# Performance work log

Hardware: AMD Instinct MI355X
Metric: run time of the kernel (lower is better)

## Reference

```python
import jax, jax.numpy as jnp
import numpy as np

NUM_EMBEDDINGS = 1024
EMBEDDING_DIM = 64
COMMITMENT_COST = 0.25


def setup_inputs() -> dict:
    key = jax.random.key(0)
    k1, k2 = jax.random.split(key)
    inputs = jax.random.normal(k1, (64, 32, 32, EMBEDDING_DIM), dtype=jnp.float32)
    # torch init is uniform(-1/K, 1/K); scale accordingly
    weight = jax.random.uniform(
        k2, (NUM_EMBEDDINGS, EMBEDDING_DIM), dtype=jnp.float32,
        minval=-1.0 / NUM_EMBEDDINGS, maxval=1.0 / NUM_EMBEDDINGS)
    return {"inputs": inputs, "weight": weight}


def reference(inputs, weight):
    input_shape = inputs.shape
    flat = inputs.reshape(-1, EMBEDDING_DIM)               # [N, D]
    distances = (jnp.sum(flat ** 2, axis=1, keepdims=True)
                 + jnp.sum(weight ** 2, axis=1)
                 - 2.0 * flat @ weight.T)                   # [N, K]
    encoding_indices = jnp.argmin(distances, axis=1)        # [N]
    # gather codes (equivalent to one-hot @ weight, but as a direct gather)
    quantized = weight[encoding_indices].reshape(input_shape)

    e_latent_loss = jnp.mean((jax.lax.stop_gradient(quantized) - inputs) ** 2)
    q_latent_loss = jnp.mean((quantized - jax.lax.stop_gradient(inputs)) ** 2)
    loss = q_latent_loss + COMMITMENT_COST * e_latent_loss

    # straight-through estimator
    quantized_ste = inputs + jax.lax.stop_gradient(quantized - inputs)

    # perplexity (equivalent to mean over the one-hot encodings)
    n_tokens = flat.shape[0]
    counts = jax.ops.segment_sum(
        jnp.ones((n_tokens,), jnp.float32), encoding_indices,
        num_segments=NUM_EMBEDDINGS)
    avg_probs = counts / n_tokens
    perplexity = jnp.exp(-jnp.sum(avg_probs * jnp.log(avg_probs + 1e-10)))

    indices_for_transformer = encoding_indices.reshape(input_shape[0], -1)
    return (loss, quantized_ste, perplexity, indices_for_transformer)
```

## Files before the change

kernel.cpp:

```cpp
#include <hip/hip_runtime.h>
#include <cstdint>
#include <cstddef>

#define N_TOKENS 65536
#define DIM 64
#define K_CODES 1024
#define NTH 256
#define NTHM 512
#define TPB 128
#define NCH 16

#define OFF_Q 1
#define OFF_PERP 4194305
#define OFF_IDX 4194306

#define MARGIN 1.5e-4f
#define HMARGIN 7.5e-5f

#define WS_LOSS   0
#define WS_FCNT   8
#define WS_COUNTS 16
#define WS_WHI    4112
#define WS_WLO    135184
#define WS_S2     266256
#define WS_FLIST  270352

typedef __attribute__((ext_vector_type(8))) short  s16x8;
typedef __attribute__((ext_vector_type(4))) float  f32x4;

__device__ __forceinline__ float fmulr(float a, float b){ return __fmul_rn(a,b); }
__device__ __forceinline__ float faddr(float a, float b){ return __fadd_rn(a,b); }

__device__ __forceinline__ unsigned short f2bf(float f) {
    unsigned u = __float_as_uint(f);
    unsigned r = u + 0x7fffu + ((u >> 16) & 1u);
    return (unsigned short)(r >> 16);
}
__device__ __forceinline__ float bf2f(unsigned short h) {
    return __uint_as_float(((unsigned)h) << 16);
}

__device__ float sumsq64_np(const float* __restrict__ p) {
    float s[16];
    #pragma unroll
    for (int l = 0; l < 16; ++l) {
        float a0 = fmulr(p[l],      p[l]);
        float a1 = fmulr(p[l + 16], p[l + 16]);
        float a2 = fmulr(p[l + 32], p[l + 32]);
        float a3 = fmulr(p[l + 48], p[l + 48]);
        s[l] = faddr(faddr(a0, a1), faddr(a2, a3));
    }
    #pragma unroll
    for (int len = 8; len >= 1; len >>= 1)
        #pragma unroll
        for (int l = 0; l < len; ++l)
            s[l] = faddr(s[l], s[l + len]);
    return s[0];
}

__device__ __forceinline__ void async_copy16(const void* g, void* l) {
    __builtin_amdgcn_global_load_lds(
        (const __attribute__((address_space(1))) void*)g,
        (__attribute__((address_space(3))) void*)l, 16, 0, 0);
}

__global__ void vq_prep(const float* __restrict__ W, unsigned short* __restrict__ Whi,
                        unsigned short* __restrict__ Wlo, float* __restrict__ s2g,
                        int* __restrict__ counts, int* __restrict__ gfcount,
                        double* __restrict__ loss_acc) {
    int gid = blockIdx.x * NTH + threadIdx.x;
    for (int e = gid; e < K_CODES * DIM; e += 16384) {
        float x = W[e];
        unsigned short hi = f2bf(x);
        unsigned short lo = f2bf(__fsub_rn(x, bf2f(hi)));
        int j = e >> 6, k = e & 63;
        int pos = j * 64 + (((k >> 3) ^ (j & 7)) << 3) + (k & 7);
        Whi[pos] = hi; Wlo[pos] = lo;
    }
    if (gid < K_CODES) { s2g[gid] = sumsq64_np(W + gid * 64); counts[gid] = 0; }
    if (gid == 0) { *loss_acc = 0.0; *gfcount = 0; }
}

__global__ __launch_bounds__(NTHM, 4)
void vq_main(const float* __restrict__ X, const float* __restrict__ W,
             const unsigned short* __restrict__ WhiG, const unsigned short* __restrict__ WloG,
             const float* __restrict__ s2g, float* __restrict__ out,
             double* __restrict__ loss_acc, int* __restrict__ counts,
             int* __restrict__ gfcount, unsigned short* __restrict__ gflist) {
    __shared__ __align__(16) unsigned short xs_hi[TPB * 64];
    __shared__ __align__(16) unsigned short xs_lo[TPB * 64];
    __shared__ __align__(16) unsigned short ws_hi[2][64 * 64];
    __shared__ __align__(16) unsigned short ws_lo[2][64 * 64];
    __shared__ __align__(16) float s2s[K_CODES];
    __shared__ float sm1[2][TPB];
    __shared__ float sm2[2][TPB];
    __shared__ int   si1[2][TPB];
    __shared__ int fidx[TPB];
    __shared__ int flist[TPB];
    __shared__ int fcount, gbaseS;
    __shared__ double lred[8];

    const int tid  = threadIdx.x;
    const int lane = tid & 63, wave = tid >> 6;
    const int quad = lane >> 4, lrow = lane & 15;
    const int tg   = wave & 3;
    const int chd  = wave >> 2;
    const int t0   = blockIdx.x * TPB;

    if (tid == 0) fcount = 0;

    {
        const char* gh = (const char*)WhiG;
        const char* gl = (const char*)WloG;
        char* lh = (char*)&ws_hi[0][0] + wave * 1024;
        char* ll = (char*)&ws_lo[0][0] + wave * 1024;
        async_copy16(gh + tid * 16, lh);
        async_copy16(gl + tid * 16, ll);
    }
    if (tid < 256) *(f32x4*)&s2s[tid * 4] = *(const f32x4*)&s2g[tid * 4];
    #pragma unroll
    for (int i = 0; i < 2; ++i) {
        int g = tid + NTHM * i;
        int t = g >> 3, kb = g & 7;
        const float* src = X + (size_t)(t0 + t) * DIM + kb * 8;
        float v[8];
        *(f32x4*)v       = *(const f32x4*)src;
        *(f32x4*)(v + 4) = *(const f32x4*)(src + 4);
        unsigned short h[8], l[8];
        #pragma unroll
        for (int k = 0; k < 8; ++k) {
            h[k] = f2bf(v[k]);
            l[k] = f2bf(__fsub_rn(v[k], bf2f(h[k])));
        }
        int base = t * 64 + ((kb ^ (t & 7)) << 3);
        *(s16x8*)&xs_hi[base] = *(s16x8*)h;
        *(s16x8*)&xs_lo[base] = *(s16x8*)l;
    }
    __syncthreads();

    s16x8 a_h0[2], a_h1[2], a_l0[2], a_l1[2];
    #pragma unroll
    for (int rt = 0; rt < 2; ++rt) {
        int tf = tg * 32 + rt * 16 + lrow;
        int sA = tf & 7;
        a_h0[rt] = *(const s16x8*)&xs_hi[tf * 64 + (((0 + quad) ^ sA) << 3)];
        a_h1[rt] = *(const s16x8*)&xs_hi[tf * 64 + (((4 + quad) ^ sA) << 3)];
        a_l0[rt] = *(const s16x8*)&xs_lo[tf * 64 + (((0 + quad) ^ sA) << 3)];
        a_l1[rt] = *(const s16x8*)&xs_lo[tf * 64 + (((4 + quad) ^ sA) << 3)];
    }

    float m1v[8], m2v[8]; int m1i[8];
    #pragma unroll
    for (int ri = 0; ri < 8; ++ri) { m1v[ri] = -3.4e38f; m2v[ri] = -3.4e38f; m1i[ri] = 0x7fffffff; }

    for (int ch = 0; ch < NCH; ++ch) {
        const int buf = ch & 1;
        if (ch < NCH - 1) {
            const char* gh = (const char*)WhiG + (ch + 1) * 8192;
            const char* gl = (const char*)WloG + (ch + 1) * 8192;
            char* lh = (char*)&ws_hi[buf ^ 1][0] + wave * 1024;
            char* ll = (char*)&ws_lo[buf ^ 1][0] + wave * 1024;
            async_copy16(gh + tid * 16, lh);
            async_copy16(gl + tid * 16, ll);
        }
        #pragma unroll
        for (int ct2 = 0; ct2 < 2; ++ct2) {
            int lc = chd * 32 + ct2 * 16 + lrow;
            int sB = lrow & 7;
            const unsigned short* bh = &ws_hi[buf][lc * 64];
            const unsigned short* bl = &ws_lo[buf][lc * 64];
            s16x8 b_h0 = *(const s16x8*)&bh[((0 + quad) ^ sB) << 3];
            s16x8 b_h1 = *(const s16x8*)&bh[((4 + quad) ^ sB) << 3];
            s16x8 b_l0 = *(const s16x8*)&bl[((0 + quad) ^ sB) << 3];
            s16x8 b_l1 = *(const s16x8*)&bl[((4 + quad) ^ sB) << 3];
            int jcode = ch * 64 + lc;
            float s2v = s2s[jcode];
            float ainit = fmulr(-0.5f, s2v);
            #pragma unroll
            for (int rt = 0; rt < 2; ++rt) {
                f32x4 acc = {ainit, ainit, ainit, ainit};
                acc = __builtin_amdgcn_mfma_f32_16x16x32_bf16(a_h0[rt], b_h0, acc, 0, 0, 0);
                acc = __builtin_amdgcn_mfma_f32_16x16x32_bf16(a_h1[rt], b_h1, acc, 0, 0, 0);
                acc = __builtin_amdgcn_mfma_f32_16x16x32_bf16(a_h0[rt], b_l0, acc, 0, 0, 0);
                acc = __builtin_amdgcn_mfma_f32_16x16x32_bf16(a_h1[rt], b_l1, acc, 0, 0, 0);
                acc = __builtin_amdgcn_mfma_f32_16x16x32_bf16(a_l0[rt], b_h0, acc, 0, 0, 0);
                acc = __builtin_amdgcn_mfma_f32_16x16x32_bf16(a_l1[rt], b_h1, acc, 0, 0, 0);
                #pragma unroll
                for (int r = 0; r < 4; ++r) {
                    float a = acc[r];
                    int ri = rt * 4 + r;
                    bool gt = a > m1v[ri];
                    float sec = gt ? m1v[ri] : a;
                    m2v[ri] = fmaxf(m2v[ri], sec);
                    m1v[ri] = gt ? a : m1v[ri];
                    m1i[ri] = gt ? jcode : m1i[ri];
                }
            }
        }
        __syncthreads();
    }

    #pragma unroll
    for (int m = 1; m <= 8; m <<= 1) {
        #pragma unroll
        for (int ri = 0; ri < 8; ++ri) {
            float o1v = __shfl_xor(m1v[ri], m, 64);
            int   o1i = __shfl_xor(m1i[ri], m, 64);
            float o2v = __shfl_xor(m2v[ri], m, 64);
            bool take = (o1v > m1v[ri]) || (o1v == m1v[ri] && o1i < m1i[ri]);
            float loser = take ? m1v[ri] : o1v;
            m2v[ri] = fmaxf(fmaxf(m2v[ri], o2v), loser);
            if (take) { m1v[ri] = o1v; m1i[ri] = o1i; }
        }
    }
    if (lrow == 0) {
        #pragma unroll
        for (int ri = 0; ri < 8; ++ri) {
            int rt = ri >> 2, r = ri & 3;
            int t = tg * 32 + rt * 16 + quad * 4 + r;
            sm1[chd][t] = m1v[ri];
            sm2[chd][t] = m2v[ri];
            si1[chd][t] = m1i[ri];
        }
    }
    __syncthreads();
    if (tid < TPB) {
        int t = tid;
        float a1 = sm1[0][t], b1 = sm1[1][t];
        int   ia = si1[0][t], ib = si1[1][t];
        float a2 = sm2[0][t], b2 = sm2[1][t];
        bool take = (b1 > a1) || (b1 == a1 && ib < ia);
        float w1 = take ? b1 : a1;
        int   wi = take ? ib : ia;
        float loser = take ? a1 : b1;
        float w2 = fmaxf(fmaxf(a2, b2), loser);
        bool fb = __fsub_rn(w1, w2) < HMARGIN;
        fidx[t] = fb ? (wi | (int)0x80000000) : wi;
        if (fb) { int p = atomicAdd(&fcount, 1); flist[p] = t; }
    }
    __syncthreads();

    double lsum = 0.0;
    #pragma unroll
    for (int i = 0; i < 4; ++i) {
        int e4 = tid + NTHM * i;
        int t = e4 >> 4, d4 = (e4 & 15) * 4;
        int iv = fidx[t];
        if (iv >= 0) {
            f32x4 q = *(const f32x4*)&W[iv * 64 + d4];
            f32x4 x = *(const f32x4*)&X[(size_t)(t0 + t) * 64 + d4];
            *(f32x4*)&out[(size_t)OFF_Q + (size_t)(t0 + t) * 64 + d4] = q;
            #pragma unroll
            for (int c = 0; c < 4; ++c) {
                float df = __fsub_rn(q[c], x[c]);
                lsum += (double)fmulr(df, df);
            }
        }
    }
    #pragma unroll
    for (int off = 32; off >= 1; off >>= 1) lsum += __shfl_down(lsum, off, 64);
    if (lane == 0) lred[wave] = lsum;
    if (tid < TPB) {
        int iv = fidx[tid];
        if (iv >= 0) {
            atomicAdd(&counts[iv], 1);
            out[(size_t)OFF_IDX + t0 + tid] = (float)iv;
        }
    }
    if (tid == 0) gbaseS = atomicAdd(gfcount, fcount);
    __syncthreads();
    if (tid < fcount) gflist[gbaseS + tid] = (unsigned short)(t0 + flist[tid]);
    if (tid == 0)
        atomicAdd(loss_acc, lred[0] + lred[1] + lred[2] + lred[3] +
                            lred[4] + lred[5] + lred[6] + lred[7]);
}

__global__ __launch_bounds__(NTH, 3)
void vq_fallback(const float* __restrict__ X, const float* __restrict__ W,
                 const float* __restrict__ s2g, const int* __restrict__ gfcount,
                 const unsigned short* __restrict__ gflist, float* __restrict__ out,
                 double* __restrict__ loss_acc, int* __restrict__ counts) {
    int count = *gfcount;
    int base = blockIdx.x * 64;
    if (base >= count) return;
    int nt = min(64, count - base);

    __shared__ __align__(16) float xsf[64 * 64];
    __shared__ __align__(16) float wsf[128 * 64];
    __shared__ float s1f[64];
    __shared__ int gidx[64];
    __shared__ double lredf[4];

    const int tid = threadIdx.x;
    const int lane = tid & 63, wave = tid >> 6;
    const int r = tid & 15, c = tid >> 4;

    #pragma unroll
    for (int i = 0; i < 4; ++i) {
        int idx = tid + NTH * i;
        int t = idx >> 4, kb = idx & 15;
        int tok = gflist[base + (t < nt ? t : 0)];
        f32x4 v = *(const f32x4*)(X + (size_t)tok * 64 + kb * 4);
        *(f32x4*)&xsf[t * 64 + ((kb ^ ((t >> 2) & 7)) << 2)] = v;
    }
    if (tid < nt) s1f[tid] = sumsq64_np(X + (size_t)gflist[base + tid] * 64);

    float runVal[4]; int runIdx[4];
    #pragma unroll
    for (int i = 0; i < 4; ++i) { runVal[i] = 3.4e38f; runIdx[i] = 0; }

    for (int ch = 0; ch < 8; ++ch) {
        __syncthreads();
        #pragma unroll
        for (int i = 0; i < 8; ++i) {
            int idx = tid + NTH * i;
            int jl = idx >> 4, kb = idx & 15;
            f32x4 v = *(const f32x4*)(W + (size_t)(ch * 128 + jl) * 64 + kb * 4);
            *(f32x4*)&wsf[jl * 64 + ((kb ^ ((jl >> 3) & 7)) << 2)] = v;
        }
        __syncthreads();

        float acc[4][8];
        #pragma unroll
        for (int i = 0; i < 4; ++i)
            #pragma unroll
            for (int m = 0; m < 8; ++m) acc[i][m] = 0.0f;

        #pragma unroll
        for (int kb = 0; kb < 16; ++kb) {
            f32x4 xv[4], wv[8];
            #pragma unroll
            for (int i = 0; i < 4; ++i)
                xv[i] = *(const f32x4*)&xsf[(4 * r + i) * 64 + ((kb ^ (r & 7)) << 2)];
            #pragma unroll
            for (int m = 0; m < 8; ++m)
                wv[m] = *(const f32x4*)&wsf[(8 * c + m) * 64 + ((kb ^ (c & 7)) << 2)];
            #pragma unroll
            for (int i = 0; i < 4; ++i)
                #pragma unroll
                for (int m = 0; m < 8; ++m) {
                    acc[i][m] = __builtin_fmaf(xv[i][0], wv[m][0], acc[i][m]);
                    acc[i][m] = __builtin_fmaf(xv[i][1], wv[m][1], acc[i][m]);
                    acc[i][m] = __builtin_fmaf(xv[i][2], wv[m][2], acc[i][m]);
                    acc[i][m] = __builtin_fmaf(xv[i][3], wv[m][3], acc[i][m]);
                }
        }
        #pragma unroll
        for (int i = 0; i < 4; ++i) {
            float s1v = s1f[4 * r + i];
            #pragma unroll
            for (int m = 0; m < 8; ++m) {
                int jl = 8 * c + m;
                float d = faddr(faddr(s1v, s2g[ch * 128 + jl]), fmulr(-2.0f, acc[i][m]));
                if (d < runVal[i]) { runVal[i] = d; runIdx[i] = ch * 128 + jl; }
            }
        }
    }

    __syncthreads();
    unsigned long long* red = (unsigned long long*)wsf;
    #pragma unroll
    for (int i = 0; i < 4; ++i) {
        unsigned long long pk =
            ((unsigned long long)__float_as_uint(runVal[i]) << 32) |
            (unsigned long long)(unsigned int)runIdx[i];
        red[(4 * r + i) * 16 + c] = pk;
    }
    __syncthreads();
    if (tid < 64) {
        unsigned long long best = red[tid * 16];
        #pragma unroll
        for (int cc = 1; cc < 16; ++cc) {
            unsigned long long v = red[tid * 16 + cc];
            best = (v < best) ? v : best;
        }
        int idx = (int)(best & 0xffffffffu);
        gidx[tid] = idx;
        if (tid < nt) {
            int tok = gflist[base + tid];
            out[(size_t)OFF_IDX + tok] = (float)idx;
            atomicAdd(&counts[idx], 1);
        }
    }
    __syncthreads();
    double lsum = 0.0;
    #pragma unroll
    for (int i = 0; i < 4; ++i) {
        int e4 = tid + NTH * i;
        int t = e4 >> 4, d4 = (e4 & 15) * 4;
        if (t < nt) {
            int tok = gflist[base + t];
            int idx = gidx[t];
            f32x4 q = *(const f32x4*)&W[idx * 64 + d4];
            f32x4 x = *(const f32x4*)&X[(size_t)tok * 64 + d4];
            *(f32x4*)&out[(size_t)OFF_Q + (size_t)tok * 64 + d4] = q;
            #pragma unroll
            for (int cc = 0; cc < 4; ++cc) {
                float df = __fsub_rn(q[cc], x[cc]);
                lsum += (double)fmulr(df, df);
            }
        }
    }
    #pragma unroll
    for (int off = 32; off >= 1; off >>= 1) lsum += __shfl_down(lsum, off, 64);
    if (lane == 0) lredf[wave] = lsum;
    __syncthreads();
    if (tid == 0) atomicAdd(loss_acc, lredf[0] + lredf[1] + lredf[2] + lredf[3]);
}

__global__ void vq_final(const int* __restrict__ counts,
                         const double* __restrict__ loss_acc,
                         float* __restrict__ out) {
    __shared__ double hred[4];
    int tid = threadIdx.x;
    double h = 0.0;
    for (int j = tid; j < K_CODES; j += 256) {
        double p = (double)counts[j] / 65536.0;
        h += p * log(p + 1e-10);
    }
    #pragma unroll
    for (int off = 32; off >= 1; off >>= 1) h += __shfl_down(h, off, 64);
    if ((tid & 63) == 0) hred[tid >> 6] = h;
    __syncthreads();
    if (tid == 0) {
        double H = hred[0] + hred[1] + hred[2] + hred[3];
        out[OFF_PERP] = (float)exp(-H);
        double ls = *loss_acc;
        float Lf = (float)(ls / 4194304.0);
        out[0] = faddr(Lf, fmulr(0.25f, Lf));
    }
}

extern "C" void kernel_launch(void* const* d_in, const int* in_sizes, int n_in,
                              void* d_out, int out_size, void* d_ws, size_t ws_size,
                              hipStream_t stream) {
    const float* X = (const float*)d_in[0];
    const float* W = (const float*)d_in[1];
    float* out = (float*)d_out;
    char* ws = (char*)d_ws;
    double* loss_acc = (double*)(ws + WS_LOSS);
    int* gfcount = (int*)(ws + WS_FCNT);
    int* counts = (int*)(ws + WS_COUNTS);
    unsigned short* Whi = (unsigned short*)(ws + WS_WHI);
    unsigned short* Wlo = (unsigned short*)(ws + WS_WLO);
    float* s2g = (float*)(ws + WS_S2);
    unsigned short* gflist = (unsigned short*)(ws + WS_FLIST);

    vq_prep<<<64, NTH, 0, stream>>>(W, Whi, Wlo, s2g, counts, gfcount, loss_acc);
    vq_main<<<N_TOKENS / TPB, NTHM, 0, stream>>>(X, W, Whi, Wlo, s2g, out,
                                                 loss_acc, counts, gfcount, gflist);
    vq_fallback<<<N_TOKENS / 64, NTH, 0, stream>>>(X, W, s2g, gfcount, gflist,
                                                   out, loss_acc, counts);
    vq_final<<<1, NTH, 0, stream>>>(counts, loss_acc, out);
}
```

Measured before the change: 166.0 us.

## Halve main-kernel tile, alias LDS, and split fallback into codebook-parallel scan plus finish

Result: slower. 300.4 us (+81.0%).

```diff
diff --git a/kernel.cpp b/kernel.cpp
--- a/kernel.cpp
+++ b/kernel.cpp
@@ -7,7 +7,7 @@
 #define K_CODES 1024
 #define NTH 256
 #define NTHM 512
-#define TPB 128
+#define TPB 64
 #define NCH 16
 
 #define OFF_Q 1
@@ -24,6 +24,7 @@
 #define WS_WLO    135184
 #define WS_S2     266256
 #define WS_FLIST  270352
+#define WS_FBBEST 401424
 
 typedef __attribute__((ext_vector_type(8))) short  s16x8;
 typedef __attribute__((ext_vector_type(4))) float  f32x4;
@@ -67,7 +68,8 @@
 __global__ void vq_prep(const float* __restrict__ W, unsigned short* __restrict__ Whi,
                         unsigned short* __restrict__ Wlo, float* __restrict__ s2g,
                         int* __restrict__ counts, int* __restrict__ gfcount,
-                        double* __restrict__ loss_acc) {
+                        double* __restrict__ loss_acc,
+                        unsigned long long* __restrict__ fbbest) {
     int gid = blockIdx.x * NTH + threadIdx.x;
     for (int e = gid; e < K_CODES * DIM; e += 16384) {
         float x = W[e];
@@ -77,51 +79,43 @@
         int pos = j * 64 + (((k >> 3) ^ (j & 7)) << 3) + (k & 7);
         Whi[pos] = hi; Wlo[pos] = lo;
     }
+    #pragma unroll
+    for (int i = 0; i < 4; ++i) fbbest[gid + 16384 * i] = ~0ULL;
     if (gid < K_CODES) { s2g[gid] = sumsq64_np(W + gid * 64); counts[gid] = 0; }
     if (gid == 0) { *loss_acc = 0.0; *gfcount = 0; }
 }
 
-__global__ __launch_bounds__(NTHM, 4)
+__global__ __launch_bounds__(NTHM, 8)
 void vq_main(const float* __restrict__ X, const float* __restrict__ W,
              const unsigned short* __restrict__ WhiG, const unsigned short* __restrict__ WloG,
              const float* __restrict__ s2g, float* __restrict__ out,
              double* __restrict__ loss_acc, int* __restrict__ counts,
              int* __restrict__ gfcount, unsigned short* __restrict__ gflist) {
-    __shared__ __align__(16) unsigned short xs_hi[TPB * 64];
-    __shared__ __align__(16) unsigned short xs_lo[TPB * 64];
-    __shared__ __align__(16) unsigned short ws_hi[2][64 * 64];
-    __shared__ __align__(16) unsigned short ws_lo[2][64 * 64];
+    __shared__ __align__(16) char uraw[32768];
     __shared__ __align__(16) float s2s[K_CODES];
-    __shared__ float sm1[2][TPB];
-    __shared__ float sm2[2][TPB];
-    __shared__ int   si1[2][TPB];
     __shared__ int fidx[TPB];
     __shared__ int flist[TPB];
     __shared__ int fcount, gbaseS;
     __shared__ double lred[8];
 
+    unsigned short* xs_hi = (unsigned short*)uraw;
+    unsigned short* xs_lo = (unsigned short*)(uraw + 16384);
+    float (*sm1)[TPB] = (float(*)[TPB])uraw;
+    float (*sm2)[TPB] = (float(*)[TPB])(uraw + 1024);
+    int   (*si1)[TPB] = (int  (*)[TPB])(uraw + 2048);
+
     const int tid  = threadIdx.x;
     const int lane = tid & 63, wave = tid >> 6;
     const int quad = lane >> 4, lrow = lane & 15;
-    const int tg   = wave & 3;
-    const int chd  = wave >> 2;
+    const int tg   = wave & 1;
+    const int chd  = wave >> 1;
     const int t0   = blockIdx.x * TPB;
 
     if (tid == 0) fcount = 0;
 
+    if (tid < 256) *(f32x4*)&s2s[tid * 4] = *(const f32x4*)&s2g[tid * 4];
     {
-        const char* gh = (const char*)WhiG;
-        const char* gl = (const char*)WloG;
-        char* lh = (char*)&ws_hi[0][0] + wave * 1024;
-        char* ll = (char*)&ws_lo[0][0] + wave * 1024;
-        async_copy16(gh + tid * 16, lh);
-        async_copy16(gl + tid * 16, ll);
-    }
-    if (tid < 256) *(f32x4*)&s2s[tid * 4] = *(const f32x4*)&s2g[tid * 4];
-    #pragma unroll
-    for (int i = 0; i < 2; ++i) {
-        int g = tid + NTHM * i;
-        int t = g >> 3, kb = g & 7;
+        int t = tid >> 3, kb = tid & 7;
         const float* src = X + (size_t)(t0 + t) * DIM + kb * 8;
         float v[8];
         *(f32x4*)v       = *(const f32x4*)src;
@@ -148,27 +142,36 @@
         a_l0[rt] = *(const s16x8*)&xs_lo[tf * 64 + (((0 + quad) ^ sA) << 3)];
         a_l1[rt] = *(const s16x8*)&xs_lo[tf * 64 + (((4 + quad) ^ sA) << 3)];
     }
+    __syncthreads();
+
+    {
+        const char* gh = (const char*)WhiG;
+        const char* gl = (const char*)WloG;
+        char* b0 = uraw + wave * 1024;
+        char* b1 = uraw + 16384 + wave * 1024;
+        async_copy16(gh + tid * 16,        b0);
+        async_copy16(gl + tid * 16,        b0 + 8192);
+        async_copy16(gh + 8192 + tid * 16, b1);
+        async_copy16(gl + 8192 + tid * 16, b1 + 8192);
+    }
 
     float m1v[8], m2v[8]; int m1i[8];
     #pragma unroll
     for (int ri = 0; ri < 8; ++ri) { m1v[ri] = -3.4e38f; m2v[ri] = -3.4e38f; m1i[ri] = 0x7fffffff; }
 
     for (int ch = 0; ch < NCH; ++ch) {
-        const int buf = ch & 1;
-        if (ch < NCH - 1) {
-            const char* gh = (const char*)WhiG + (ch + 1) * 8192;
-            const char* gl = (const char*)WloG + (ch + 1) * 8192;
-            char* lh = (char*)&ws_hi[buf ^ 1][0] + wave * 1024;
-            char* ll = (char*)&ws_lo[buf ^ 1][0] + wave * 1024;
-            async_copy16(gh + tid * 16, lh);
-            async_copy16(gl + tid * 16, ll);
-        }
-        #pragma unroll
-        for (int ct2 = 0; ct2 < 2; ++ct2) {
-            int lc = chd * 32 + ct2 * 16 + lrow;
+        if (ch < NCH - 1) asm volatile("s_waitcnt vmcnt(2)" ::: "memory");
+        else              asm volatile("s_waitcnt vmcnt(0)" ::: "memory");
+        __builtin_amdgcn_s_barrier();
+        __builtin_amdgcn_sched_barrier(0);
+
+        const unsigned short* wh = (const unsigned short*)(uraw + (ch & 1) * 16384);
+        const unsigned short* wl = wh + 4096;
+        {
+            int lc = chd * 16 + lrow;
             int sB = lrow & 7;
-            const unsigned short* bh = &ws_hi[buf][lc * 64];
-            const unsigned short* bl = &ws_lo[buf][lc * 64];
+            const unsigned short* bh = &wh[lc * 64];
+            const unsigned short* bl = &wl[lc * 64];
             s16x8 b_h0 = *(const s16x8*)&bh[((0 + quad) ^ sB) << 3];
             s16x8 b_h1 = *(const s16x8*)&bh[((4 + quad) ^ sB) << 3];
             s16x8 b_l0 = *(const s16x8*)&bl[((0 + quad) ^ sB) << 3];
@@ -197,7 +200,17 @@
                 }
             }
         }
-        __syncthreads();
+
+        __builtin_amdgcn_sched_barrier(0);
+        __builtin_amdgcn_s_barrier();
+        __builtin_amdgcn_sched_barrier(0);
+        if (ch + 2 < NCH) {
+            const char* gh = (const char*)WhiG + (ch + 2) * 8192;
+            const char* gl = (const char*)WloG + (ch + 2) * 8192;
+            char* lb = uraw + (ch & 1) * 16384 + wave * 1024;
+            async_copy16(gh + tid * 16, lb);
+            async_copy16(gl + tid * 16, lb + 8192);
+        }
     }
 
     #pragma unroll
@@ -226,14 +239,16 @@
     __syncthreads();
     if (tid < TPB) {
         int t = tid;
-        float a1 = sm1[0][t], b1 = sm1[1][t];
-        int   ia = si1[0][t], ib = si1[1][t];
-        float a2 = sm2[0][t], b2 = sm2[1][t];
-        bool take = (b1 > a1) || (b1 == a1 && ib < ia);
-        float w1 = take ? b1 : a1;
-        int   wi = take ? ib : ia;
-        float loser = take ? a1 : b1;
-        float w2 = fmaxf(fmaxf(a2, b2), loser);
+        float w1 = sm1[0][t], w2 = sm2[0][t];
+        int   wi = si1[0][t];
+        #pragma unroll
+        for (int h = 1; h < 4; ++h) {
+            float c1 = sm1[h][t]; int ci = si1[h][t];
+            bool take = (c1 > w1) || (c1 == w1 && ci < wi);
+            float loser = take ? w1 : c1;
+            if (take) { w1 = c1; wi = ci; }
+            w2 = fmaxf(fmaxf(w2, sm2[h][t]), loser);
+        }
         bool fb = __fsub_rn(w1, w2) < HMARGIN;
         fidx[t] = fb ? (wi | (int)0x80000000) : wi;
         if (fb) { int p = atomicAdd(&fcount, 1); flist[p] = t; }
@@ -242,7 +257,7 @@
 
     double lsum = 0.0;
     #pragma unroll
-    for (int i = 0; i < 4; ++i) {
+    for (int i = 0; i < 2; ++i) {
         int e4 = tid + NTHM * i;
         int t = e4 >> 4, d4 = (e4 & 15) * 4;
         int iv = fidx[t];
@@ -276,48 +291,43 @@
 }
 
 __global__ __launch_bounds__(NTH, 3)
-void vq_fallback(const float* __restrict__ X, const float* __restrict__ W,
-                 const float* __restrict__ s2g, const int* __restrict__ gfcount,
-                 const unsigned short* __restrict__ gflist, float* __restrict__ out,
-                 double* __restrict__ loss_acc, int* __restrict__ counts) {
+void vq_fb_scan(const float* __restrict__ X, const float* __restrict__ W,
+                const float* __restrict__ s2g, const int* __restrict__ gfcount,
+                const unsigned short* __restrict__ gflist,
+                unsigned long long* __restrict__ fbbest) {
     int count = *gfcount;
-    int base = blockIdx.x * 64;
-    if (base >= count) return;
-    int nt = min(64, count - base);
+    if (count <= 0) return;
+    int nunits = ((count + 63) >> 6) << 3;
 
     __shared__ __align__(16) float xsf[64 * 64];
     __shared__ __align__(16) float wsf[128 * 64];
     __shared__ float s1f[64];
-    __shared__ int gidx[64];
-    __shared__ double lredf[4];
 
     const int tid = threadIdx.x;
-    const int lane = tid & 63, wave = tid >> 6;
     const int r = tid & 15, c = tid >> 4;
 
-    #pragma unroll
-    for (int i = 0; i < 4; ++i) {
-        int idx = tid + NTH * i;
-        int t = idx >> 4, kb = idx & 15;
-        int tok = gflist[base + (t < nt ? t : 0)];
-        f32x4 v = *(const f32x4*)(X + (size_t)tok * 64 + kb * 4);
-        *(f32x4*)&xsf[t * 64 + ((kb ^ ((t >> 2) & 7)) << 2)] = v;
-    }
-    if (tid < nt) s1f[tid] = sumsq64_np(X + (size_t)gflist[base + tid] * 64);
-
-    float runVal[4]; int runIdx[4];
-    #pragma unroll
-    for (int i = 0; i < 4; ++i) { runVal[i] = 3.4e38f; runIdx[i] = 0; }
-
-    for (int ch = 0; ch < 8; ++ch) {
+    for (int u = blockIdx.x; u < nunits; u += 1024) {
+        int bt = u >> 3, bc = u & 7;
+        int base = bt << 6;
+        int nt = min(64, count - base);
         __syncthreads();
+
+        #pragma unroll
+        for (int i = 0; i < 4; ++i) {
+            int idx = tid + NTH * i;
+            int t = idx >> 4, kb = idx & 15;
+            int tok = gflist[base + (t < nt ? t : 0)];
+            f32x4 v = *(const f32x4*)(X + (size_t)tok * 64 + kb * 4);
+            *(f32x4*)&xsf[t * 64 + ((kb ^ ((t >> 2) & 7)) << 2)] = v;
+        }
         #pragma unroll
         for (int i = 0; i < 8; ++i) {
             int idx = tid + NTH * i;
             int jl = idx >> 4, kb = idx & 15;
-            f32x4 v = *(const f32x4*)(W + (size_t)(ch * 128 + jl) * 64 + kb * 4);
+            f32x4 v = *(const f32x4*)(W + (size_t)(bc * 128 + jl) * 64 + kb * 4);
             *(f32x4*)&wsf[jl * 64 + ((kb ^ ((jl >> 3) & 7)) << 2)] = v;
         }
+        if (tid < nt) s1f[tid] = sumsq64_np(X + (size_t)gflist[base + tid] * 64);
         __syncthreads();
 
         float acc[4][8];
@@ -345,67 +355,78 @@
                     acc[i][m] = __builtin_fmaf(xv[i][3], wv[m][3], acc[i][m]);
                 }
         }
+        float runVal[4]; int runIdx[4];
+        #pragma unroll
+        for (int i = 0; i < 4; ++i) { runVal[i] = 3.4e38f; runIdx[i] = 0; }
         #pragma unroll
         for (int i = 0; i < 4; ++i) {
             float s1v = s1f[4 * r + i];
             #pragma unroll
             for (int m = 0; m < 8; ++m) {
                 int jl = 8 * c + m;
-                float d = faddr(faddr(s1v, s2g[ch * 128 + jl]), fmulr(-2.0f, acc[i][m]));
-                if (d < runVal[i]) { runVal[i] = d; runIdx[i] = ch * 128 + jl; }
+                float d = faddr(faddr(s1v, s2g[bc * 128 + jl]), fmulr(-2.0f, acc[i][m]));
+                if (d < runVal[i]) { runVal[i] = d; runIdx[i] = bc * 128 + jl; }
             }
         }
-    }
-
-    __syncthreads();
-    unsigned long long* red = (unsigned long long*)wsf;
-    #pragma unroll
-    for (int i = 0; i < 4; ++i) {
-        unsigned long long pk =
-            ((unsigned long long)__float_as_uint(runVal[i]) << 32) |
-            (unsigned long long)(unsigned int)runIdx[i];
-        red[(4 * r + i) * 16 + c] = pk;
-    }
-    __syncthreads();
-    if (tid < 64) {
-        unsigned long long best = red[tid * 16];
-        #pragma unroll
-        for (int cc = 1; cc < 16; ++cc) {
-            unsigned long long v = red[tid * 16 + cc];
-            best = (v < best) ? v : best;
-        }
-        int idx = (int)(best & 0xffffffffu);
-        gidx[tid] = idx;
+
+        __syncthreads();
+        unsigned long long* red = (unsigned long long*)wsf;
+        #pragma unroll
+        for (int i = 0; i < 4; ++i) {
+            unsigned long long pk =
+                ((unsigned long long)__float_as_uint(runVal[i]) << 32) |
+                (unsigned long long)(unsigned int)runIdx[i];
+            red[(4 * r + i) * 16 + c] = pk;
+        }
+        __syncthreads();
         if (tid < nt) {
-            int tok = gflist[base + tid];
+            unsigned long long best = red[tid * 16];
+            #pragma unroll
+            for (int cc = 1; cc < 16; ++cc) {
+                unsigned long long v = red[tid * 16 + cc];
+                best = (v < best) ? v : best;
+            }
+            atomicMin(&fbbest[base + tid], best);
+        }
+    }
+}
+
+__global__ __launch_bounds__(NTH, 4)
+void vq_fb_fin(const float* __restrict__ X, const float* __restrict__ W,
+               const int* __restrict__ gfcount, const unsigned short* __restrict__ gflist,
+               const unsigned long long* __restrict__ fbbest, float* __restrict__ out,
+               double* __restrict__ loss_acc, int* __restrict__ counts) {
+    int count = *gfcount;
+    __shared__ double lred[4];
+    const int tid = threadIdx.x;
+    const int lane = tid & 63, wave = tid >> 6;
+    double lsum = 0.0;
+    int total = count << 4;
+    for (int g = blockIdx.x * NTH + tid; g < total; g += NTH * 256) {
+        int p = g >> 4, d4 = (g & 15) << 2;
+        int tok = gflist[p];
+        int idx = (int)(fbbest[p] & 0xffffffffULL);
+        f32x4 q = *(const f32x4*)&W[idx * 64 + d4];
+        f32x4 x = *(const f32x4*)&X[(size_t)tok * 64 + d4];
+        *(f32x4*)&out[(size_t)OFF_Q + (size_t)tok * 64 + d4] = q;
+        #pragma unroll
+        for (int cc = 0; cc < 4; ++cc) {
+            float df = __fsub_rn(q[cc], x[cc]);
+            lsum += (double)fmulr(df, df);
+        }
+        if ((g & 15) == 0) {
             out[(size_t)OFF_IDX + tok] = (float)idx;
             atomicAdd(&counts[idx], 1);
         }
     }
-    __syncthreads();
-    double lsum = 0.0;
-    #pragma unroll
-    for (int i = 0; i < 4; ++i) {
-        int e4 = tid + NTH * i;
-        int t = e4 >> 4, d4 = (e4 & 15) * 4;
-        if (t < nt) {
-            int tok = gflist[base + t];
-            int idx = gidx[t];
-            f32x4 q = *(const f32x4*)&W[idx * 64 + d4];
-            f32x4 x = *(const f32x4*)&X[(size_t)tok * 64 + d4];
-            *(f32x4*)&out[(size_t)OFF_Q + (size_t)tok * 64 + d4] = q;
-            #pragma unroll
-            for (int cc = 0; cc < 4; ++cc) {
-                float df = __fsub_rn(q[cc], x[cc]);
-                lsum += (double)fmulr(df, df);
-            }
-        }
-    }
     #pragma unroll
     for (int off = 32; off >= 1; off >>= 1) lsum += __shfl_down(lsum, off, 64);
-    if (lane == 0) lredf[wave] = lsum;
-    __syncthreads();
-    if (tid == 0) atomicAdd(loss_acc, lredf[0] + lredf[1] + lredf[2] + lredf[3]);
+    if (lane == 0) lred[wave] = lsum;
+    __syncthreads();
+    if (tid == 0) {
+        double t = lred[0] + lred[1] + lred[2] + lred[3];
+        if (t != 0.0) atomicAdd(loss_acc, t);
+    }
 }
 
 __global__ void vq_final(const int* __restrict__ counts,
@@ -445,11 +466,13 @@
     unsigned short* Wlo = (unsigned short*)(ws + WS_WLO);
     float* s2g = (float*)(ws + WS_S2);
     unsigned short* gflist = (unsigned short*)(ws + WS_FLIST);
-
-    vq_prep<<<64, NTH, 0, stream>>>(W, Whi, Wlo, s2g, counts, gfcount, loss_acc);
+    unsigned long long* fbbest = (unsigned long long*)(ws + WS_FBBEST);
+
+    vq_prep<<<64, NTH, 0, stream>>>(W, Whi, Wlo, s2g, counts, gfcount, loss_acc, fbbest);
     vq_main<<<N_TOKENS / TPB, NTHM, 0, stream>>>(X, W, Whi, Wlo, s2g, out,
                                                  loss_acc, counts, gfcount, gflist);
-    vq_fallback<<<N_TOKENS / 64, NTH, 0, stream>>>(X, W, s2g, gfcount, gflist,
-                                                   out, loss_acc, counts);
+    vq_fb_scan<<<1024, NTH, 0, stream>>>(X, W, s2g, gfcount, gflist, fbbest);
+    vq_fb_fin<<<256, NTH, 0, stream>>>(X, W, gfcount, gflist, fbbest, out,
+                                       loss_acc, counts);
     vq_final<<<1, NTH, 0, stream>>>(counts, loss_acc, out);
 }
```

## Track top-two candidates and resolve near-ties locally with exact fp32 dot products

Applied to the files above, without the earlier changes.

Result: slower. 232.3 us (+39.9%).

```diff
diff --git a/kernel.cpp b/kernel.cpp
--- a/kernel.cpp
+++ b/kernel.cpp
@@ -56,6 +56,21 @@
         for (int l = 0; l < len; ++l)
             s[l] = faddr(s[l], s[l + len]);
     return s[0];
+}
+
+__device__ __forceinline__ float exact_dot64(const float* __restrict__ x,
+                                             const float* __restrict__ w) {
+    float acc = 0.0f;
+    #pragma unroll
+    for (int kb = 0; kb < 16; ++kb) {
+        f32x4 xv = *(const f32x4*)(x + kb * 4);
+        f32x4 wv = *(const f32x4*)(w + kb * 4);
+        acc = __builtin_fmaf(xv[0], wv[0], acc);
+        acc = __builtin_fmaf(xv[1], wv[1], acc);
+        acc = __builtin_fmaf(xv[2], wv[2], acc);
+        acc = __builtin_fmaf(xv[3], wv[3], acc);
+    }
+    return acc;
 }
 
 __device__ __forceinline__ void async_copy16(const void* g, void* l) {
@@ -94,7 +109,9 @@
     __shared__ __align__(16) float s2s[K_CODES];
     __shared__ float sm1[2][TPB];
     __shared__ float sm2[2][TPB];
+    __shared__ float sm3[2][TPB];
     __shared__ int   si1[2][TPB];
+    __shared__ int   si2[2][TPB];
     __shared__ int fidx[TPB];
     __shared__ int flist[TPB];
     __shared__ int fcount, gbaseS;
@@ -149,9 +166,12 @@
         a_l1[rt] = *(const s16x8*)&xs_lo[tf * 64 + (((4 + quad) ^ sA) << 3)];
     }
 
-    float m1v[8], m2v[8]; int m1i[8];
-    #pragma unroll
-    for (int ri = 0; ri < 8; ++ri) { m1v[ri] = -3.4e38f; m2v[ri] = -3.4e38f; m1i[ri] = 0x7fffffff; }
+    float m1v[8], m2v[8], m3v[8]; int m1i[8], m2i[8];
+    #pragma unroll
+    for (int ri = 0; ri < 8; ++ri) {
+        m1v[ri] = -3.4e38f; m2v[ri] = -3.4e38f; m3v[ri] = -3.4e38f;
+        m1i[ri] = 0x7fffffff; m2i[ri] = 0x7fffffff;
+    }
 
     for (int ch = 0; ch < NCH; ++ch) {
         const int buf = ch & 1;
@@ -189,11 +209,14 @@
                 for (int r = 0; r < 4; ++r) {
                     float a = acc[r];
                     int ri = rt * 4 + r;
-                    bool gt = a > m1v[ri];
-                    float sec = gt ? m1v[ri] : a;
-                    m2v[ri] = fmaxf(m2v[ri], sec);
-                    m1v[ri] = gt ? a : m1v[ri];
-                    m1i[ri] = gt ? jcode : m1i[ri];
+                    bool gt1 = a > m1v[ri];
+                    bool gt2 = a > m2v[ri];
+                    bool gt3 = a > m3v[ri];
+                    m3v[ri] = gt2 ? m2v[ri] : (gt3 ? a : m3v[ri]);
+                    m2i[ri] = gt1 ? m1i[ri] : (gt2 ? jcode : m2i[ri]);
+                    m2v[ri] = gt1 ? m1v[ri] : (gt2 ? a : m2v[ri]);
+                    m1i[ri] = gt1 ? jcode : m1i[ri];
+                    m1v[ri] = gt1 ? a : m1v[ri];
                 }
             }
         }
@@ -204,13 +227,25 @@
     for (int m = 1; m <= 8; m <<= 1) {
         #pragma unroll
         for (int ri = 0; ri < 8; ++ri) {
-            float o1v = __shfl_xor(m1v[ri], m, 64);
-            int   o1i = __shfl_xor(m1i[ri], m, 64);
-            float o2v = __shfl_xor(m2v[ri], m, 64);
-            bool take = (o1v > m1v[ri]) || (o1v == m1v[ri] && o1i < m1i[ri]);
-            float loser = take ? m1v[ri] : o1v;
-            m2v[ri] = fmaxf(fmaxf(m2v[ri], o2v), loser);
-            if (take) { m1v[ri] = o1v; m1i[ri] = o1i; }
+            float o1 = __shfl_xor(m1v[ri], m, 64);
+            int  oi1 = __shfl_xor(m1i[ri], m, 64);
+            float o2 = __shfl_xor(m2v[ri], m, 64);
+            int  oi2 = __shfl_xor(m2i[ri], m, 64);
+            float o3 = __shfl_xor(m3v[ri], m, 64);
+            bool b1 = (o1 > m1v[ri]) || (o1 == m1v[ri] && oi1 < m1i[ri]);
+            bool b2 = !b1 && ((o1 > m2v[ri]) || (o1 == m2v[ri] && oi1 < m2i[ri]));
+            float t3 = (b1 || b2) ? m2v[ri] : fmaxf(m3v[ri], o1);
+            float t2v = b1 ? m1v[ri] : (b2 ? o1 : m2v[ri]);
+            int   t2i = b1 ? m1i[ri] : (b2 ? oi1 : m2i[ri]);
+            float t1v = b1 ? o1 : m1v[ri];
+            int   t1i = b1 ? oi1 : m1i[ri];
+            bool c2 = (o2 > t2v) || (o2 == t2v && oi2 < t2i);
+            float u3 = c2 ? t2v : fmaxf(t3, o2);
+            float u2v = c2 ? o2 : t2v;
+            int   u2i = c2 ? oi2 : t2i;
+            m1v[ri] = t1v; m1i[ri] = t1i;
+            m2v[ri] = u2v; m2i[ri] = u2i;
+            m3v[ri] = fmaxf(u3, o3);
         }
     }
     if (lrow == 0) {
@@ -220,23 +255,49 @@
             int t = tg * 32 + rt * 16 + quad * 4 + r;
             sm1[chd][t] = m1v[ri];
             sm2[chd][t] = m2v[ri];
+            sm3[chd][t] = m3v[ri];
             si1[chd][t] = m1i[ri];
+            si2[chd][t] = m2i[ri];
         }
     }
     __syncthreads();
     if (tid < TPB) {
         int t = tid;
-        float a1 = sm1[0][t], b1 = sm1[1][t];
-        int   ia = si1[0][t], ib = si1[1][t];
-        float a2 = sm2[0][t], b2 = sm2[1][t];
-        bool take = (b1 > a1) || (b1 == a1 && ib < ia);
-        float w1 = take ? b1 : a1;
-        int   wi = take ? ib : ia;
-        float loser = take ? a1 : b1;
-        float w2 = fmaxf(fmaxf(a2, b2), loser);
-        bool fb = __fsub_rn(w1, w2) < HMARGIN;
-        fidx[t] = fb ? (wi | (int)0x80000000) : wi;
-        if (fb) { int p = atomicAdd(&fcount, 1); flist[p] = t; }
+        float w1 = sm1[0][t], w2 = sm2[0][t], w3 = sm3[0][t];
+        int   i1 = si1[0][t], i2 = si2[0][t];
+        float o1 = sm1[1][t], o2 = sm2[1][t], o3 = sm3[1][t];
+        int  oi1 = si1[1][t], oi2 = si2[1][t];
+        bool b1 = (o1 > w1) || (o1 == w1 && oi1 < i1);
+        bool b2 = !b1 && ((o1 > w2) || (o1 == w2 && oi1 < i2));
+        float t3 = (b1 || b2) ? w2 : fmaxf(w3, o1);
+        float t2v = b1 ? w1 : (b2 ? o1 : w2);
+        int   t2i = b1 ? i1 : (b2 ? oi1 : i2);
+        float t1v = b1 ? o1 : w1;
+        int   t1i = b1 ? oi1 : i1;
+        bool c2 = (o2 > t2v) || (o2 == t2v && oi2 < t2i);
+        float u3 = c2 ? t2v : fmaxf(t3, o2);
+        float u2v = c2 ? o2 : t2v;
+        int   u2i = c2 ? oi2 : t2i;
+        w1 = t1v; i1 = t1i; w2 = u2v; i2 = u2i; w3 = fmaxf(u3, o3);
+
+        float d12 = __fsub_rn(w1, w2);
+        float d13 = __fsub_rn(w1, w3);
+        int v;
+        if (d12 >= HMARGIN) {
+            v = i1;
+        } else if (d13 > HMARGIN) {
+            const float* xr = X + (size_t)(t0 + t) * 64;
+            float s1 = sumsq64_np(xr);
+            float accA = exact_dot64(xr, W + (size_t)i1 * 64);
+            float accB = exact_dot64(xr, W + (size_t)i2 * 64);
+            float dA = faddr(faddr(s1, s2s[i1]), fmulr(-2.0f, accA));
+            float dB = faddr(faddr(s1, s2s[i2]), fmulr(-2.0f, accB));
+            v = ((dB < dA) || (dB == dA && i2 < i1)) ? i2 : i1;
+        } else {
+            v = i1 | (int)0x80000000;
+            int p = atomicAdd(&fcount, 1); flist[p] = t;
+        }
+        fidx[t] = v;
     }
     __syncthreads();
 
```

## Fuse fallback refinement and final scalars into main VQ kernel

Applied to the files above, without the earlier changes.

Result: slower. 211.9 us (+27.6%).

```diff
diff --git a/kernel.cpp b/kernel.cpp
--- a/kernel.cpp
+++ b/kernel.cpp
@@ -9,6 +9,7 @@
 #define NTHM 512
 #define TPB 128
 #define NCH 16
+#define NBLK (N_TOKENS / TPB)
 
 #define OFF_Q 1
 #define OFF_PERP 4194305
@@ -18,12 +19,11 @@
 #define HMARGIN 7.5e-5f
 
 #define WS_LOSS   0
-#define WS_FCNT   8
+#define WS_TICKET 8
 #define WS_COUNTS 16
 #define WS_WHI    4112
 #define WS_WLO    135184
 #define WS_S2     266256
-#define WS_FLIST  270352
 
 typedef __attribute__((ext_vector_type(8))) short  s16x8;
 typedef __attribute__((ext_vector_type(4))) float  f32x4;
@@ -66,7 +66,7 @@
 
 __global__ void vq_prep(const float* __restrict__ W, unsigned short* __restrict__ Whi,
                         unsigned short* __restrict__ Wlo, float* __restrict__ s2g,
-                        int* __restrict__ counts, int* __restrict__ gfcount,
+                        int* __restrict__ counts, int* __restrict__ ticket,
                         double* __restrict__ loss_acc) {
     int gid = blockIdx.x * NTH + threadIdx.x;
     for (int e = gid; e < K_CODES * DIM; e += 16384) {
@@ -78,27 +78,51 @@
         Whi[pos] = hi; Wlo[pos] = lo;
     }
     if (gid < K_CODES) { s2g[gid] = sumsq64_np(W + gid * 64); counts[gid] = 0; }
-    if (gid == 0) { *loss_acc = 0.0; *gfcount = 0; }
-}
-
-__global__ __launch_bounds__(NTHM, 4)
+    if (gid == 0) { *loss_acc = 0.0; *ticket = 0; }
+}
+
+__device__ void final_scalars(int* __restrict__ counts, double* __restrict__ loss_acc,
+                              float* __restrict__ out, int tid, double* hred) {
+    double h = 0.0;
+    for (int j = tid; j < K_CODES; j += NTHM) {
+        int cj = atomicAdd(&counts[j], 0);
+        double p = (double)cj / 65536.0;
+        h += p * log(p + 1e-10);
+    }
+    #pragma unroll
+    for (int off = 32; off >= 1; off >>= 1) h += __shfl_down(h, off, 64);
+    if ((tid & 63) == 0) hred[tid >> 6] = h;
+    __syncthreads();
+    if (tid == 0) {
+        double H = 0.0;
+        #pragma unroll
+        for (int w = 0; w < 8; ++w) H += hred[w];
+        out[OFF_PERP] = (float)exp(-H);
+        double ls = atomicAdd(loss_acc, 0.0);
+        float Lf = (float)(ls / 4194304.0);
+        out[0] = faddr(Lf, fmulr(0.25f, Lf));
+    }
+}
+
+__global__ __launch_bounds__(NTHM, 2)
 void vq_main(const float* __restrict__ X, const float* __restrict__ W,
              const unsigned short* __restrict__ WhiG, const unsigned short* __restrict__ WloG,
              const float* __restrict__ s2g, float* __restrict__ out,
              double* __restrict__ loss_acc, int* __restrict__ counts,
-             int* __restrict__ gfcount, unsigned short* __restrict__ gflist) {
-    __shared__ __align__(16) unsigned short xs_hi[TPB * 64];
-    __shared__ __align__(16) unsigned short xs_lo[TPB * 64];
-    __shared__ __align__(16) unsigned short ws_hi[2][64 * 64];
-    __shared__ __align__(16) unsigned short ws_lo[2][64 * 64];
+             int* __restrict__ ticket) {
+    __shared__ __align__(16) char uA[32768];
+    __shared__ __align__(16) char uB[32768];
     __shared__ __align__(16) float s2s[K_CODES];
     __shared__ float sm1[2][TPB];
     __shared__ float sm2[2][TPB];
     __shared__ int   si1[2][TPB];
     __shared__ int fidx[TPB];
     __shared__ int flist[TPB];
-    __shared__ int fcount, gbaseS;
+    __shared__ int fcount, lastflag;
     __shared__ double lred[8];
+
+    unsigned short* xs_hi = (unsigned short*)uA;
+    unsigned short* xs_lo = (unsigned short*)(uA + 16384);
 
     const int tid  = threadIdx.x;
     const int lane = tid & 63, wave = tid >> 6;
@@ -112,8 +136,8 @@
     {
         const char* gh = (const char*)WhiG;
         const char* gl = (const char*)WloG;
-        char* lh = (char*)&ws_hi[0][0] + wave * 1024;
-        char* ll = (char*)&ws_lo[0][0] + wave * 1024;
+        char* lh = uB + wave * 1024;
+        char* ll = uB + 16384 + wave * 1024;
         async_copy16(gh + tid * 16, lh);
         async_copy16(gl + tid * 16, ll);
     }
@@ -158,17 +182,19 @@
         if (ch < NCH - 1) {
             const char* gh = (const char*)WhiG + (ch + 1) * 8192;
             const char* gl = (const char*)WloG + (ch + 1) * 8192;
-            char* lh = (char*)&ws_hi[buf ^ 1][0] + wave * 1024;
-            char* ll = (char*)&ws_lo[buf ^ 1][0] + wave * 1024;
+            char* lh = uB + (buf ^ 1) * 8192 + wave * 1024;
+            char* ll = uB + 16384 + (buf ^ 1) * 8192 + wave * 1024;
             async_copy16(gh + tid * 16, lh);
             async_copy16(gl + tid * 16, ll);
         }
+        const unsigned short* wh = (const unsigned short*)(uB + buf * 8192);
+        const unsigned short* wl = (const unsigned short*)(uB + 16384 + buf * 8192);
         #pragma unroll
         for (int ct2 = 0; ct2 < 2; ++ct2) {
             int lc = chd * 32 + ct2 * 16 + lrow;
             int sB = lrow & 7;
-            const unsigned short* bh = &ws_hi[buf][lc * 64];
-            const unsigned short* bl = &ws_lo[buf][lc * 64];
+            const unsigned short* bh = &wh[lc * 64];
+            const unsigned short* bl = &wl[lc * 64];
             s16x8 b_h0 = *(const s16x8*)&bh[((0 + quad) ^ sB) << 3];
             s16x8 b_h1 = *(const s16x8*)&bh[((4 + quad) ^ sB) << 3];
             s16x8 b_l0 = *(const s16x8*)&bl[((0 + quad) ^ sB) << 3];
@@ -257,9 +283,6 @@
             }
         }
     }
-    #pragma unroll
-    for (int off = 32; off >= 1; off >>= 1) lsum += __shfl_down(lsum, off, 64);
-    if (lane == 0) lred[wave] = lsum;
     if (tid < TPB) {
         int iv = fidx[tid];
         if (iv >= 0) {
@@ -267,167 +290,101 @@
             out[(size_t)OFF_IDX + t0 + tid] = (float)iv;
         }
     }
-    if (tid == 0) gbaseS = atomicAdd(gfcount, fcount);
-    __syncthreads();
-    if (tid < fcount) gflist[gbaseS + tid] = (unsigned short)(t0 + flist[tid]);
-    if (tid == 0)
-        atomicAdd(loss_acc, lred[0] + lred[1] + lred[2] + lred[3] +
-                            lred[4] + lred[5] + lred[6] + lred[7]);
-}
-
-__global__ __launch_bounds__(NTH, 3)
-void vq_fallback(const float* __restrict__ X, const float* __restrict__ W,
-                 const float* __restrict__ s2g, const int* __restrict__ gfcount,
-                 const unsigned short* __restrict__ gflist, float* __restrict__ out,
-                 double* __restrict__ loss_acc, int* __restrict__ counts) {
-    int count = *gfcount;
-    int base = blockIdx.x * 64;
-    if (base >= count) return;
-    int nt = min(64, count - base);
-
-    __shared__ __align__(16) float xsf[64 * 64];
-    __shared__ __align__(16) float wsf[128 * 64];
-    __shared__ float s1f[64];
-    __shared__ int gidx[64];
-    __shared__ double lredf[4];
-
-    const int tid = threadIdx.x;
-    const int lane = tid & 63, wave = tid >> 6;
-    const int r = tid & 15, c = tid >> 4;
-
-    #pragma unroll
-    for (int i = 0; i < 4; ++i) {
-        int idx = tid + NTH * i;
-        int t = idx >> 4, kb = idx & 15;
-        int tok = gflist[base + (t < nt ? t : 0)];
-        f32x4 v = *(const f32x4*)(X + (size_t)tok * 64 + kb * 4);
-        *(f32x4*)&xsf[t * 64 + ((kb ^ ((t >> 2) & 7)) << 2)] = v;
-    }
-    if (tid < nt) s1f[tid] = sumsq64_np(X + (size_t)gflist[base + tid] * 64);
-
-    float runVal[4]; int runIdx[4];
-    #pragma unroll
-    for (int i = 0; i < 4; ++i) { runVal[i] = 3.4e38f; runIdx[i] = 0; }
-
-    for (int ch = 0; ch < 8; ++ch) {
+
+    const int fc = fcount;
+    if (fc > 0) {
+        float* xsr = (float*)uB;
+        float* wck = (float*)uA;
+        unsigned long long* tbest = (unsigned long long*)sm1;
+        float* s1f = (float*)sm2;
+        for (int g = tid; g < fc * 16; g += NTHM) {
+            int ti = g >> 4, kb = g & 15;
+            int tok = t0 + flist[ti];
+            *(f32x4*)&xsr[ti * 64 + kb * 4] =
+                *(const f32x4*)&X[(size_t)tok * 64 + kb * 4];
+        }
+        if (tid < fc) {
+            tbest[tid] = ~0ULL;
+            s1f[tid] = sumsq64_np(X + (size_t)(t0 + flist[tid]) * 64);
+        }
         __syncthreads();
-        #pragma unroll
-        for (int i = 0; i < 8; ++i) {
-            int idx = tid + NTH * i;
-            int jl = idx >> 4, kb = idx & 15;
-            f32x4 v = *(const f32x4*)(W + (size_t)(ch * 128 + jl) * 64 + kb * 4);
-            *(f32x4*)&wsf[jl * 64 + ((kb ^ ((jl >> 3) & 7)) << 2)] = v;
+        for (int ch = 0; ch < NCH; ++ch) {
+            #pragma unroll
+            for (int i = 0; i < 2; ++i) {
+                int g = tid + NTHM * i;
+                int jl = g >> 4, kb = g & 15;
+                f32x4 v = *(const f32x4*)&W[(size_t)(ch * 64 + jl) * 64 + kb * 4];
+                *(f32x4*)&wck[jl * 64 + ((kb ^ ((jl >> 3) & 7)) << 2)] = v;
+            }
+            __syncthreads();
+            for (int p = tid; p < fc * 64; p += NTHM) {
+                int ti = p >> 6, c = p & 63;
+                float acc = 0.0f;
+                #pragma unroll
+                for (int kb = 0; kb < 16; ++kb) {
+                    f32x4 xv = *(const f32x4*)&xsr[ti * 64 + kb * 4];
+                    f32x4 wv = *(const f32x4*)&wck[c * 64 + ((kb ^ ((c >> 3) & 7)) << 2)];
+                    acc = __builtin_fmaf(xv[0], wv[0], acc);
+                    acc = __builtin_fmaf(xv[1], wv[1], acc);
+                    acc = __builtin_fmaf(xv[2], wv[2], acc);
+                    acc = __builtin_fmaf(xv[3], wv[3], acc);
+                }
+                int j = ch * 64 + c;
+                float d = faddr(faddr(s1f[ti], s2s[j]), fmulr(-2.0f, acc));
+                unsigned long long pk =
+                    ((unsigned long long)__float_as_uint(d) << 32) |
+                    (unsigned long long)(unsigned int)j;
+                #pragma unroll
+                for (int m = 32; m >= 1; m >>= 1) {
+                    unsigned long long o =
+                        ((unsigned long long)(unsigned)__shfl_xor((int)(pk >> 32), m, 64) << 32) |
+                        (unsigned long long)(unsigned)__shfl_xor((int)(pk & 0xffffffffu), m, 64);
+                    pk = (o < pk) ? o : pk;
+                }
+                if (lane == 0) atomicMin(&tbest[ti], pk);
+            }
+            __syncthreads();
+        }
+        if (tid < fc) {
+            int idx = (int)(tbest[tid] & 0xffffffffu);
+            int t = flist[tid];
+            fidx[t] = idx;
+            out[(size_t)OFF_IDX + t0 + t] = (float)idx;
+            atomicAdd(&counts[idx], 1);
         }
         __syncthreads();
-
-        float acc[4][8];
-        #pragma unroll
-        for (int i = 0; i < 4; ++i)
+        for (int g = tid; g < fc * 16; g += NTHM) {
+            int ti = g >> 4, d4 = (g & 15) * 4;
+            int t = flist[ti];
+            int idx = fidx[t];
+            f32x4 q = *(const f32x4*)&W[idx * 64 + d4];
+            f32x4 x = *(const f32x4*)&xsr[ti * 64 + d4];
+            *(f32x4*)&out[(size_t)OFF_Q + (size_t)(t0 + t) * 64 + d4] = q;
             #pragma unroll
-            for (int m = 0; m < 8; ++m) acc[i][m] = 0.0f;
-
-        #pragma unroll
-        for (int kb = 0; kb < 16; ++kb) {
-            f32x4 xv[4], wv[8];
-            #pragma unroll
-            for (int i = 0; i < 4; ++i)
-                xv[i] = *(const f32x4*)&xsf[(4 * r + i) * 64 + ((kb ^ (r & 7)) << 2)];
-            #pragma unroll
-            for (int m = 0; m < 8; ++m)
-                wv[m] = *(const f32x4*)&wsf[(8 * c + m) * 64 + ((kb ^ (c & 7)) << 2)];
-            #pragma unroll
-            for (int i = 0; i < 4; ++i)
-                #pragma unroll
-                for (int m = 0; m < 8; ++m) {
-                    acc[i][m] = __builtin_fmaf(xv[i][0], wv[m][0], acc[i][m]);
-                    acc[i][m] = __builtin_fmaf(xv[i][1], wv[m][1], acc[i][m]);
-                    acc[i][m] = __builtin_fmaf(xv[i][2], wv[m][2], acc[i][m]);
-                    acc[i][m] = __builtin_fmaf(xv[i][3], wv[m][3], acc[i][m]);
-                }
-        }
-        #pragma unroll
-        for (int i = 0; i < 4; ++i) {
-            float s1v = s1f[4 * r + i];
-            #pragma unroll
-            for (int m = 0; m < 8; ++m) {
-                int jl = 8 * c + m;
-                float d = faddr(faddr(s1v, s2g[ch * 128 + jl]), fmulr(-2.0f, acc[i][m]));
-                if (d < runVal[i]) { runVal[i] = d; runIdx[i] = ch * 128 + jl; }
-            }
-        }
-    }
-
-    __syncthreads();
-    unsigned long long* red = (unsigned long long*)wsf;
-    #pragma unroll
-    for (int i = 0; i < 4; ++i) {
-        unsigned long long pk =
-            ((unsigned long long)__float_as_uint(runVal[i]) << 32) |
-            (unsigned long long)(unsigned int)runIdx[i];
-        red[(4 * r + i) * 16 + c] = pk;
-    }
-    __syncthreads();
-    if (tid < 64) {
-        unsigned long long best = red[tid * 16];
-        #pragma unroll
-        for (int cc = 1; cc < 16; ++cc) {
-            unsigned long long v = red[tid * 16 + cc];
-            best = (v < best) ? v : best;
-        }
-        int idx = (int)(best & 0xffffffffu);
-        gidx[tid] = idx;
-        if (tid < nt) {
-            int tok = gflist[base + tid];
-            out[(size_t)OFF_IDX + tok] = (float)idx;
-            atomicAdd(&counts[idx], 1);
-        }
-    }
-    __syncthreads();
-    double lsum = 0.0;
-    #pragma unroll
-    for (int i = 0; i < 4; ++i) {
-        int e4 = tid + NTH * i;
-        int t = e4 >> 4, d4 = (e4 & 15) * 4;
-        if (t < nt) {
-            int tok = gflist[base + t];
-            int idx = gidx[t];
-            f32x4 q = *(const f32x4*)&W[idx * 64 + d4];
-            f32x4 x = *(const f32x4*)&X[(size_t)tok * 64 + d4];
-            *(f32x4*)&out[(size_t)OFF_Q + (size_t)tok * 64 + d4] = q;
-            #pragma unroll
-            for (int cc = 0; cc < 4; ++cc) {
-                float df = __fsub_rn(q[cc], x[cc]);
+            for (int c = 0; c < 4; ++c) {
+                float df = __fsub_rn(q[c], x[c]);
                 lsum += (double)fmulr(df, df);
             }
         }
     }
+
     #pragma unroll
     for (int off = 32; off >= 1; off >>= 1) lsum += __shfl_down(lsum, off, 64);
-    if (lane == 0) lredf[wave] = lsum;
-    __syncthreads();
-    if (tid == 0) atomicAdd(loss_acc, lredf[0] + lredf[1] + lredf[2] + lredf[3]);
-}
-
-__global__ void vq_final(const int* __restrict__ counts,
-                         const double* __restrict__ loss_acc,
-                         float* __restrict__ out) {
-    __shared__ double hred[4];
-    int tid = threadIdx.x;
-    double h = 0.0;
-    for (int j = tid; j < K_CODES; j += 256) {
-        double p = (double)counts[j] / 65536.0;
-        h += p * log(p + 1e-10);
-    }
-    #pragma unroll
-    for (int off = 32; off >= 1; off >>= 1) h += __shfl_down(h, off, 64);
-    if ((tid & 63) == 0) hred[tid >> 6] = h;
+    if (lane == 0) lred[wave] = lsum;
     __syncthreads();
     if (tid == 0) {
-        double H = hred[0] + hred[1] + hred[2] + hred[3];
-        out[OFF_PERP] = (float)exp(-H);
-        double ls = *loss_acc;
-        float Lf = (float)(ls / 4194304.0);
-        out[0] = faddr(Lf, fmulr(0.25f, Lf));
+        double s = 0.0;
+        #pragma unroll
+        for (int w = 0; w < 8; ++w) s += lred[w];
+        atomicAdd(loss_acc, s);
+    }
+    __threadfence();
+    __syncthreads();
+    if (tid == 0) lastflag = (atomicAdd(ticket, 1) == NBLK - 1);
+    __syncthreads();
+    if (lastflag) {
+        __threadfence();
+        final_scalars(counts, loss_acc, out, tid, lred);
     }
 }
 
@@ -439,17 +396,13 @@
     float* out = (float*)d_out;
     char* ws = (char*)d_ws;
     double* loss_acc = (double*)(ws + WS_LOSS);
-    int* gfcount = (int*)(ws + WS_FCNT);
+    int* ticket = (int*)(ws + WS_TICKET);
     int* counts = (int*)(ws + WS_COUNTS);
     unsigned short* Whi = (unsigned short*)(ws + WS_WHI);
     unsigned short* Wlo = (unsigned short*)(ws + WS_WLO);
     float* s2g = (float*)(ws + WS_S2);
-    unsigned short* gflist = (unsigned short*)(ws + WS_FLIST);
-
-    vq_prep<<<64, NTH, 0, stream>>>(W, Whi, Wlo, s2g, counts, gfcount, loss_acc);
-    vq_main<<<N_TOKENS / TPB, NTHM, 0, stream>>>(X, W, Whi, Wlo, s2g, out,
-                                                 loss_acc, counts, gfcount, gflist);
-    vq_fallback<<<N_TOKENS / 64, NTH, 0, stream>>>(X, W, s2g, gfcount, gflist,
-                                                   out, loss_acc, counts);
-    vq_final<<<1, NTH, 0, stream>>>(counts, loss_acc, out);
-}
+
+    vq_prep<<<64, NTH, 0, stream>>>(W, Whi, Wlo, s2g, counts, ticket, loss_acc);
+    vq_main<<<NBLK, NTHM, 0, stream>>>(X, W, Whi, Wlo, s2g, out,
+                                       loss_acc, counts, ticket);
+}
```
